# Kernel optimization log

Hardware: AMD Instinct MI355X
Metric: run time of the kernel (lower is better)

Reference implementation:

```python
import jax, jax.numpy as jnp
import numpy as np

NEG = -1e30
EPS = 1e-10


def setup_inputs() -> dict:
    key = jax.random.key(0)
    ks = jax.random.split(key, 8)
    N, D, W = 200000, 256, 128
    B = 64
    s = 0.02  # keep linear outputs well-scaled
    return {
        "node_features": jax.random.normal(ks[0], (N, D), jnp.float32),
        "node_tiers": jax.random.randint(ks[1], (N,), 0, 3, jnp.int32),
        "query": jax.random.normal(ks[2], (B, D), jnp.float32),
        "W_mu": jax.random.normal(ks[3], (W, D), jnp.float32) * s,
        "b_mu": jnp.zeros((W,), jnp.float32),
        "W_lv": jax.random.normal(ks[4], (W, D), jnp.float32) * s,
        "b_lv": jnp.zeros((W,), jnp.float32),
        "W_dec": jax.random.normal(ks[5], (D, W), jnp.float32) * s,
        "b_dec": jnp.zeros((D,), jnp.float32),
        "top_k": 16,
    }


def reference(node_features, node_tiers, query, W_mu, b_mu, W_lv, b_lv, W_dec, b_dec, top_k):
    # tiers: 0=hot, 1=warm, 2=cold
    warm = node_tiers == 1            # [N]
    cold = node_tiers == 2            # [N]

    # --- compress_warm_nodes (eval mode: z = mu) ---
    mu = node_features @ W_mu.T + b_mu          # [N, W]
    logvar = node_features @ W_lv.T + b_lv      # [N, W]
    dec = mu @ W_dec.T + b_dec                  # [N, D]
    new_features = jnp.where(warm[:, None], dec, node_features)

    kl_terms = -0.5 * (1.0 + logvar - mu * mu - jnp.exp(logvar))  # [N, W]
    n_warm = jnp.maximum(jnp.sum(warm), 1)
    kl_loss = jnp.sum(jnp.where(warm[:, None], kl_terms, 0.0)) / (n_warm * kl_terms.shape[1])

    # --- retrieve_from_cold: cosine sim + topk + gather ---
    qn = query / (jnp.linalg.norm(query, axis=-1, keepdims=True) + EPS)          # [B, D]
    fn = new_features / (jnp.linalg.norm(new_features, axis=-1, keepdims=True) + EPS)  # [N, D]
    sim = qn @ fn.T                                                              # [B, N]
    sim = jnp.where(cold[None, :], sim, NEG)
    top_sim, top_idx = jax.lax.top_k(sim, top_k)                                 # [B, k]
    retrieved = new_features[top_idx]                                            # [B, k, D]

    return new_features, kl_loss, retrieved, top_idx
```

## Files before the change

### kernel.cpp

```cpp
#include <hip/hip_runtime.h>
#include <math.h>

#define D 256
#define WDIM 128
#define EPSN 1e-10f
#define CHUNK 2048
#define C2 2048

typedef __attribute__((ext_vector_type(8))) short short8v;
typedef __attribute__((ext_vector_type(4))) float f32x4;

#define XPAD 264
#define MPAD 136

__device__ __forceinline__ unsigned short bf16_rne(float f) {
    unsigned u = __float_as_uint(f);
    u += 0x7fffu + ((u >> 16) & 1u);
    return (unsigned short)(u >> 16);
}
__device__ __forceinline__ float bf16_tof(unsigned short h) {
    return __uint_as_float(((unsigned)h) << 16);
}
__device__ __forceinline__ void split2(float f, unsigned short& h, unsigned short& l) {
    h = bf16_rne(f);
    l = bf16_rne(f - bf16_tof(h));
}

__global__ void k_init(int* cnt) {
    if (threadIdx.x == 0) { cnt[0] = 0; cnt[1] = 0; ((float*)cnt)[2] = 0.0f; }
}

__global__ __launch_bounds__(256) void k_wconv(const float* __restrict__ Wmu,
                                               const float* __restrict__ Wlv,
                                               const float* __restrict__ Wdec,
                                               unsigned short* __restrict__ wcat_h,
                                               unsigned short* __restrict__ wcat_l,
                                               unsigned short* __restrict__ wdec_h,
                                               unsigned short* __restrict__ wdec_l) {
    int i = blockIdx.x * 256 + threadIdx.x;
    if (i < 65536) {
        float v = (i < 32768) ? Wmu[i] : Wlv[i - 32768];
        unsigned short h, l; split2(v, h, l);
        wcat_h[i] = h; wcat_l[i] = l;
    } else if (i < 98304) {
        int j = i - 65536;
        unsigned short h, l; split2(Wdec[j], h, l);
        wdec_h[j] = h; wdec_l[j] = l;
    }
}

__global__ __launch_bounds__(256) void k_copy_norm(const float* __restrict__ x,
                                                   float* __restrict__ outF,
                                                   float* __restrict__ rowinv, int N) {
    int wid = threadIdx.x >> 6, lane = threadIdx.x & 63;
    int row = blockIdx.x * 4 + wid;
    if (row >= N) return;
    float4 v = ((const float4*)(x + (size_t)row * D))[lane];
    ((float4*)(outF + (size_t)row * D))[lane] = v;
    float s = v.x * v.x + v.y * v.y + v.z * v.z + v.w * v.w;
    #pragma unroll
    for (int m = 32; m; m >>= 1) s += __shfl_xor(s, m, 64);
    if (lane == 0) rowinv[row] = 1.0f / (sqrtf(s) + EPSN);
}

__global__ __launch_bounds__(256) void k_classify(const int* __restrict__ tiers, int* cnt,
                                                  int* __restrict__ warm_idx,
                                                  int* __restrict__ cold_idx, int N) {
    int i = blockIdx.x * 256 + threadIdx.x;
    bool w = false, c = false;
    if (i < N) { int t = tiers[i]; w = (t == 1); c = (t == 2); }
    unsigned long long mw = __ballot(w);
    unsigned long long mc = __ballot(c);
    int lane = threadIdx.x & 63;
    unsigned long long ltmask = (lane == 0) ? 0ULL : (~0ULL >> (64 - lane));
    int pw = __popcll(mw & ltmask);
    int pc = __popcll(mc & ltmask);
    int cw = __popcll(mw), cc = __popcll(mc);
    int bw = 0, bc = 0;
    if (lane == 0) {
        if (cw) bw = atomicAdd(&cnt[0], cw);
        if (cc) bc = atomicAdd(&cnt[1], cc);
    }
    bw = __shfl(bw, 0, 64);
    bc = __shfl(bc, 0, 64);
    if (w) warm_idx[bw + pw] = i;
    if (c) cold_idx[bc + pc] = i;
}

__global__ __launch_bounds__(256) void k_qnorm(const float* __restrict__ q,
                                               float* __restrict__ qn, int B) {
    int wid = threadIdx.x >> 6, lane = threadIdx.x & 63;
    int row = blockIdx.x * 4 + wid;
    if (row >= B) return;
    float4 v = ((const float4*)(q + (size_t)row * D))[lane];
    float s = v.x * v.x + v.y * v.y + v.z * v.z + v.w * v.w;
    #pragma unroll
    for (int m = 32; m; m >>= 1) s += __shfl_xor(s, m, 64);
    float inv = 1.0f / (sqrtf(s) + EPSN);
    float4 o = make_float4(v.x * inv, v.y * inv, v.z * inv, v.w * inv);
    ((float4*)(qn + (size_t)row * D))[lane] = o;
}

__global__ __launch_bounds__(256) void k_warm(const float* __restrict__ x,
        const unsigned short* __restrict__ wcat_h, const unsigned short* __restrict__ wcat_l,
        const unsigned short* __restrict__ wdec_h, const unsigned short* __restrict__ wdec_l,
        const float* __restrict__ bmu, const float* __restrict__ blv,
        const float* __restrict__ bdec,
        const int* __restrict__ warm_idx, const int* cnt,
        float* __restrict__ outF, float* klacc) {
    __shared__ __align__(16) unsigned short SM[2 * 64 * XPAD];
    __shared__ float klbuf[4];
    unsigned short* XH = SM;
    unsigned short* XL = SM + 64 * XPAD;
    int nw = cnt[0];
    int base = blockIdx.x * 64;
    if (base >= nw) return;
    int m = min(64, nw - base);
    int tid = threadIdx.x;
    for (int i = tid; i < 64 * 64; i += 256) {
        int r = i >> 6, c4 = i & 63;
        float4 v = make_float4(0.f, 0.f, 0.f, 0.f);
        if (r < m) v = ((const float4*)(x + (size_t)warm_idx[base + r] * D))[c4];
        unsigned short h0, h1, h2, h3, l0, l1, l2, l3;
        split2(v.x, h0, l0); split2(v.y, h1, l1); split2(v.z, h2, l2); split2(v.w, h3, l3);
        *(ushort4*)&XH[r * XPAD + c4 * 4] = make_ushort4(h0, h1, h2, h3);
        *(ushort4*)&XL[r * XPAD + c4 * 4] = make_ushort4(l0, l1, l2, l3);
    }
    __syncthreads();

    int w = tid >> 6, lane = tid & 63;
    int lm = lane & 15, lk = (lane >> 4) * 8;
    int rowbase = w * 16;
    f32x4 zero; zero[0] = 0.f; zero[1] = 0.f; zero[2] = 0.f; zero[3] = 0.f;

    f32x4 acc[16];
    #pragma unroll
    for (int n = 0; n < 16; ++n) acc[n] = zero;
    const unsigned short* ah_p = &XH[(rowbase + lm) * XPAD];
    const unsigned short* al_p = &XL[(rowbase + lm) * XPAD];
    for (int ks = 0; ks < 8; ++ks) {
        int kk = ks * 32 + lk;
        short8v ah = *(const short8v*)&ah_p[kk];
        short8v al = *(const short8v*)&al_p[kk];
        #pragma unroll
        for (int n = 0; n < 16; ++n) {
            size_t roff = ((size_t)(n * 16 + lm) << 8) + kk;
            short8v bh = *(const short8v*)(wcat_h + roff);
            short8v bl = *(const short8v*)(wcat_l + roff);
            acc[n] = __builtin_amdgcn_mfma_f32_16x16x32_bf16(ah, bh, acc[n], 0, 0, 0);
            acc[n] = __builtin_amdgcn_mfma_f32_16x16x32_bf16(al, bh, acc[n], 0, 0, 0);
            acc[n] = __builtin_amdgcn_mfma_f32_16x16x32_bf16(ah, bl, acc[n], 0, 0, 0);
        }
    }

    float kll = 0.f;
    int r4 = (lane >> 4) * 4;
    #pragma unroll
    for (int n = 0; n < 8; ++n) {
        float bm = bmu[n * 16 + lm];
        float bl_ = blv[n * 16 + lm];
        #pragma unroll
        for (int rg = 0; rg < 4; ++rg) {
            float mu = acc[n][rg] + bm;
            float lv = acc[n + 8][rg] + bl_;
            acc[n][rg] = mu;
            int rl = rowbase + r4 + rg;
            if (rl < m) kll += -0.5f * (1.f + lv - mu * mu - __expf(lv));
        }
    }
    #pragma unroll
    for (int s = 32; s; s >>= 1) kll += __shfl_xor(kll, s, 64);
    if (lane == 0) klbuf[w] = kll;
    __syncthreads();
    if (tid == 0) atomicAdd(klacc, klbuf[0] + klbuf[1] + klbuf[2] + klbuf[3]);

    unsigned short* MUH = SM;
    unsigned short* MUL = SM + 64 * MPAD;
    #pragma unroll
    for (int n = 0; n < 8; ++n) {
        #pragma unroll
        for (int rg = 0; rg < 4; ++rg) {
            int rl = rowbase + r4 + rg;
            unsigned short h, l;
            split2(acc[n][rg], h, l);
            MUH[rl * MPAD + n * 16 + lm] = h;
            MUL[rl * MPAD + n * 16 + lm] = l;
        }
    }
    __syncthreads();

    f32x4 acc2[16];
    #pragma unroll
    for (int n = 0; n < 16; ++n) acc2[n] = zero;
    const unsigned short* mh_p = &MUH[(rowbase + lm) * MPAD];
    const unsigned short* ml_p = &MUL[(rowbase + lm) * MPAD];
    for (int ks = 0; ks < 4; ++ks) {
        int kk = ks * 32 + lk;
        short8v ah = *(const short8v*)&mh_p[kk];
        short8v al = *(const short8v*)&ml_p[kk];
        #pragma unroll
        for (int n = 0; n < 16; ++n) {
            size_t roff = (size_t)(n * 16 + lm) * WDIM + kk;
            short8v bh = *(const short8v*)(wdec_h + roff);
            short8v bl = *(const short8v*)(wdec_l + roff);
            acc2[n] = __builtin_amdgcn_mfma_f32_16x16x32_bf16(ah, bh, acc2[n], 0, 0, 0);
            acc2[n] = __builtin_amdgcn_mfma_f32_16x16x32_bf16(al, bh, acc2[n], 0, 0, 0);
            acc2[n] = __builtin_amdgcn_mfma_f32_16x16x32_bf16(ah, bl, acc2[n], 0, 0, 0);
        }
    }

    int gidx[4];
    #pragma unroll
    for (int rg = 0; rg < 4; ++rg) {
        int rl = rowbase + r4 + rg;
        gidx[rg] = (rl < m) ? warm_idx[base + rl] : -1;
    }
    #pragma unroll
    for (int n = 0; n < 16; ++n) {
        float bd = bdec[n * 16 + lm];
        #pragma unroll
        for (int rg = 0; rg < 4; ++rg) {
            if (gidx[rg] >= 0)
                outF[(size_t)gidx[rg] * D + n * 16 + lm] = acc2[n][rg] + bd;
        }
    }
}

__global__ __launch_bounds__(256) void k_sim(const float* __restrict__ x,
                                             const float* __restrict__ qn,
                                             const int* __restrict__ cold_idx,
                                             const float* __restrict__ rowinv, const int* cnt,
                                             float* __restrict__ simC) {
    __shared__ float xs[64][256];
    int nc = cnt[1];
    int base = blockIdx.x * 64;
    if (base >= nc) return;
    int m = min(64, nc - base);
    int tid = threadIdx.x;
    for (int i = tid; i < 64 * 64; i += 256) {
        int r = i >> 6, c4 = i & 63;
        float4 v = make_float4(0.f, 0.f, 0.f, 0.f);
        if (r < m) v = ((const float4*)(x + (size_t)cold_idx[base + r] * D))[c4];
        *(float4*)&xs[r][c4 * 4] = v;
    }
    __syncthreads();
    int qg = tid & 15, rg = tid >> 4;
    int q0 = qg * 4, r0 = rg * 4;
    float acc[4][4] = {{0}};
    for (int k4 = 0; k4 < 64; ++k4) {
        float4 xv[4];
        #pragma unroll
        for (int i = 0; i < 4; ++i) xv[i] = *(const float4*)&xs[r0 + i][k4 * 4];
        #pragma unroll
        for (int j = 0; j < 4; ++j) {
            float4 qv = ((const float4*)(qn + (size_t)(q0 + j) * D))[k4];
            #pragma unroll
            for (int i = 0; i < 4; ++i)
                acc[i][j] += xv[i].x * qv.x + xv[i].y * qv.y + xv[i].z * qv.z + xv[i].w * qv.w;
        }
    }
    #pragma unroll
    for (int i = 0; i < 4; ++i) {
        int r = r0 + i;
        if (r < m) {
            float inv = rowinv[cold_idx[base + r]];
            #pragma unroll
            for (int j = 0; j < 4; ++j)
                simC[(size_t)(q0 + j) * nc + base + r] = acc[i][j] * inv;
        }
    }
}

__device__ __forceinline__ unsigned long long mkkey(float v, int gi) {
    unsigned int b = __float_as_uint(v);
    b = (b & 0x80000000u) ? ~b : (b | 0x80000000u);
    return ((unsigned long long)b << 32) | (unsigned int)(~gi);
}

#define CE(a, b) { unsigned long long _hi = (a) >= (b) ? (a) : (b); \
                   unsigned long long _lo = (a) >= (b) ? (b) : (a); \
                   (a) = _hi; (b) = _lo; }

__global__ __launch_bounds__(256) void k_top1(const float* __restrict__ simC,
                                              const int* __restrict__ cold_idx,
                                              const int* cnt, int Mmax,
                                              unsigned long long* __restrict__ cand) {
    __shared__ unsigned long long P0[256 * 17];
    __shared__ unsigned long long P1[128 * 17];
    int nc = cnt[1];
    int c = blockIdx.x, q = blockIdx.y;
    int base = c * CHUNK;
    if (base >= nc) return;
    int tid = threadIdx.x;
    const float* srow = simC + (size_t)q * nc;
    #define LOADK(s) ((base + tid + (s)*256 < nc) \
        ? mkkey(srow[base + tid + (s)*256], cold_idx[base + tid + (s)*256]) : 0ULL)
    unsigned long long k0 = LOADK(0), k1 = LOADK(1), k2 = LOADK(2), k3 = LOADK(3);
    unsigned long long k4 = LOADK(4), k5 = LOADK(5), k6 = LOADK(6), k7 = LOADK(7);
    #undef LOADK
    CE(k0,k1) CE(k2,k3) CE(k4,k5) CE(k6,k7)
    CE(k0,k2) CE(k1,k3) CE(k4,k6) CE(k5,k7)
    CE(k1,k2) CE(k5,k6)
    CE(k0,k4) CE(k1,k5) CE(k2,k6) CE(k3,k7)
    CE(k2,k4) CE(k3,k5)
    CE(k1,k2) CE(k3,k4) CE(k5,k6)
    unsigned long long* L = P0 + tid * 17;
    L[0]=k0; L[1]=k1; L[2]=k2; L[3]=k3; L[4]=k4; L[5]=k5; L[6]=k6; L[7]=k7;
    L[8]=0; L[9]=0; L[10]=0; L[11]=0; L[12]=0; L[13]=0; L[14]=0; L[15]=0;
    __syncthreads();
    unsigned long long* src = P0;
    unsigned long long* dst = P1;
    int nl = 256;
    while (nl > 1) {
        int half = nl >> 1;
        if (tid < half) {
            unsigned long long* A  = src + (2 * tid) * 17;
            unsigned long long* Bp = src + (2 * tid + 1) * 17;
            unsigned long long* O  = dst + tid * 17;
            int i = 0, j = 0;
            #pragma unroll
            for (int t = 0; t < 16; ++t) {
                unsigned long long ka = A[i], kb = Bp[j];
                bool ta = ka >= kb;
                O[t] = ta ? ka : kb;
                i += ta ? 1 : 0;
                j += ta ? 0 : 1;
            }
        }
        __syncthreads();
        unsigned long long* tmp = src; src = dst; dst = tmp;
        nl = half;
    }
    if (tid < 16) cand[((size_t)q * Mmax + c) * 16 + tid] = src[tid];
}

__global__ __launch_bounds__(256) void k_top2(const unsigned long long* __restrict__ cand,
                                              const int* cnt, int Mmax,
                                              const float* __restrict__ newF,
                                              float* __restrict__ outRetr,
                                              float* __restrict__ outIdx) {
    __shared__ unsigned long long K[C2];
    int q = blockIdx.x, tid = threadIdx.x;
    int nc = cnt[1];
    int M = (nc + CHUNK - 1) / CHUNK; if (M > Mmax) M = Mmax;
    int C = M * 16;
    for (int i = tid; i < C2; i += 256)
        K[i] = (i < C) ? cand[(size_t)q * Mmax * 16 + i] : 0ULL;
    __syncthreads();
    for (int kk = 2; kk <= C2; kk <<= 1) {
        for (int jj = kk >> 1; jj > 0; jj >>= 1) {
            for (int idx = tid; idx < C2; idx += 256) {
                int p = idx ^ jj;
                if (p > idx) {
                    bool dirDesc = ((idx & kk) == 0);
                    unsigned long long a = K[idx], b = K[p];
                    bool sw = dirDesc ? (a < b) : (a > b);
                    if (sw) { K[idx] = b; K[p] = a; }
                }
            }
            __syncthreads();
        }
    }
    if (tid < 16) {
        int gi = (int)(~(unsigned int)(K[tid] & 0xffffffffULL));
        outIdx[q * 16 + tid] = (float)gi;
    }
    for (int i = tid; i < 16 * D; i += 256) {
        int r = i >> 8, cc = i & 255;
        int gi = (int)(~(unsigned int)(K[r] & 0xffffffffULL));
        outRetr[(size_t)q * 16 * D + i] = newF[(size_t)gi * D + cc];
    }
}

__global__ void k_klfin(const int* cnt, float* outKl, int Wk) {
    float kl = ((const float*)cnt)[2];
    int nw = cnt[0]; if (nw < 1) nw = 1;
    *outKl = kl / ((float)nw * (float)Wk);
}

extern "C" void kernel_launch(void* const* d_in, const int* in_sizes, int n_in,
                              void* d_out, int out_size, void* d_ws, size_t ws_size,
                              hipStream_t stream) {
    (void)n_in; (void)out_size; (void)ws_size;
    const float* x    = (const float*)d_in[0];
    const int*   tier = (const int*)d_in[1];
    const float* qry  = (const float*)d_in[2];
    const float* Wmu  = (const float*)d_in[3];
    const float* bmu  = (const float*)d_in[4];
    const float* Wlv  = (const float*)d_in[5];
    const float* blv  = (const float*)d_in[6];
    const float* Wdec = (const float*)d_in[7];
    const float* bdec = (const float*)d_in[8];
    int N = in_sizes[0] / D;
    int B = in_sizes[2] / D;
    int Wk = in_sizes[4];
    int Mmax = (N + CHUNK - 1) / CHUNK;

    float* outF    = (float*)d_out;
    float* outKl   = outF + (size_t)N * D;
    float* outRetr = outKl + 1;
    float* outIdx  = outRetr + (size_t)B * 16 * D;

    char* ws = (char*)d_ws;
    int*   cnt      = (int*)ws;
    int*   warm_idx = (int*)(ws + 256);
    int*   cold_idx = warm_idx + N;
    float* rowinv   = (float*)(cold_idx + N);
    float* qn       = rowinv + N;
    unsigned long long* cand = (unsigned long long*)(qn + (size_t)B * D);
    unsigned short* wcat_h = (unsigned short*)(cand + (size_t)B * Mmax * 16);
    unsigned short* wcat_l = wcat_h + 256 * 256;
    unsigned short* wdec_h = wcat_l + 256 * 256;
    unsigned short* wdec_l = wdec_h + 256 * WDIM;
    float* simC     = (float*)(wdec_l + 256 * WDIM);

    k_init<<<1, 64, 0, stream>>>(cnt);
    k_wconv<<<384, 256, 0, stream>>>(Wmu, Wlv, Wdec, wcat_h, wcat_l, wdec_h, wdec_l);
    k_copy_norm<<<(N + 3) / 4, 256, 0, stream>>>(x, outF, rowinv, N);
    k_classify<<<(N + 255) / 256, 256, 0, stream>>>(tier, cnt, warm_idx, cold_idx, N);
    k_qnorm<<<(B + 3) / 4, 256, 0, stream>>>(qry, qn, B);
    k_warm<<<(N + 63) / 64, 256, 0, stream>>>(x, wcat_h, wcat_l, wdec_h, wdec_l,
                                              bmu, blv, bdec, warm_idx, cnt,
                                              outF, (float*)cnt + 2);
    k_sim<<<(N + 63) / 64, 256, 0, stream>>>(x, qn, cold_idx, rowinv, cnt, simC);
    k_top1<<<dim3(Mmax, B), 256, 0, stream>>>(simC, cold_idx, cnt, Mmax, cand);
    k_top2<<<B, 256, 0, stream>>>(cand, cnt, Mmax, outF, outRetr, outIdx);
    k_klfin<<<1, 1, 0, stream>>>(cnt, outKl, Wk);
}
```

Baseline: 1.010 ms.

## Repartition warm VAE GEMM across waves by output columns with fragment-packed weights

Each wave in the warm-node kernel used to cover 16 rows and all output columns, so every wave loaded the full weight matrices from global memory. Now each wave covers all 64 rows but only a quarter of the output column tiles, which cuts per-block weight traffic by four. The weights are pre-packed into MFMA fragment order so each lane loads them with one coalesced 16-byte read. Warm indices are cached in shared memory for the scatter. The cost is more LDS reads of the A operand per wave and a more complex layout in the weight-conversion kernel.

New measurement: 845.9 us. 1.19x faster.

```diff
diff --git a/kernel.cpp b/kernel.cpp
--- a/kernel.cpp
+++ b/kernel.cpp
@@ -39,12 +39,18 @@
                                                unsigned short* __restrict__ wdec_l) {
     int i = blockIdx.x * 256 + threadIdx.x;
     if (i < 65536) {
-        float v = (i < 32768) ? Wmu[i] : Wlv[i - 32768];
+        int e = i & 7, lane = (i >> 3) & 63, ks = (i >> 9) & 7, n = i >> 12;
+        int row = n * 16 + (lane & 15);
+        int k = ks * 32 + ((lane >> 4) << 3) + e;
+        float v = (row < 128) ? Wmu[row * 256 + k] : Wlv[(row - 128) * 256 + k];
         unsigned short h, l; split2(v, h, l);
         wcat_h[i] = h; wcat_l[i] = l;
     } else if (i < 98304) {
         int j = i - 65536;
-        unsigned short h, l; split2(Wdec[j], h, l);
+        int e = j & 7, lane = (j >> 3) & 63, ks = (j >> 9) & 3, n = j >> 11;
+        int row = n * 16 + (lane & 15);
+        int k = ks * 32 + ((lane >> 4) << 3) + e;
+        unsigned short h, l; split2(Wdec[row * 128 + k], h, l);
         wdec_h[j] = h; wdec_l[j] = l;
     }
 }
@@ -110,6 +116,7 @@
         float* __restrict__ outF, float* klacc) {
     __shared__ __align__(16) unsigned short SM[2 * 64 * XPAD];
     __shared__ float klbuf[4];
+    __shared__ int widx[64];
     unsigned short* XH = SM;
     unsigned short* XL = SM + 64 * XPAD;
     int nw = cnt[0];
@@ -117,6 +124,7 @@
     if (base >= nw) return;
     int m = min(64, nw - base);
     int tid = threadIdx.x;
+    if (tid < 64) widx[tid] = (tid < m) ? warm_idx[base + tid] : -1;
     for (int i = tid; i < 64 * 64; i += 256) {
         int r = i >> 6, c4 = i & 63;
         float4 v = make_float4(0.f, 0.f, 0.f, 0.f);
@@ -129,43 +137,53 @@
     __syncthreads();
 
     int w = tid >> 6, lane = tid & 63;
-    int lm = lane & 15, lk = (lane >> 4) * 8;
-    int rowbase = w * 16;
+    int lm = lane & 15, hi = lane >> 4;
+    int lk = hi * 8, r4 = hi * 4;
     f32x4 zero; zero[0] = 0.f; zero[1] = 0.f; zero[2] = 0.f; zero[3] = 0.f;
 
-    f32x4 acc[16];
-    #pragma unroll
-    for (int n = 0; n < 16; ++n) acc[n] = zero;
-    const unsigned short* ah_p = &XH[(rowbase + lm) * XPAD];
-    const unsigned short* al_p = &XL[(rowbase + lm) * XPAD];
+    f32x4 acc[4][4];
+    #pragma unroll
+    for (int t = 0; t < 4; ++t)
+        #pragma unroll
+        for (int j = 0; j < 4; ++j) acc[t][j] = zero;
     for (int ks = 0; ks < 8; ++ks) {
         int kk = ks * 32 + lk;
-        short8v ah = *(const short8v*)&ah_p[kk];
-        short8v al = *(const short8v*)&al_p[kk];
-        #pragma unroll
-        for (int n = 0; n < 16; ++n) {
-            size_t roff = ((size_t)(n * 16 + lm) << 8) + kk;
-            short8v bh = *(const short8v*)(wcat_h + roff);
-            short8v bl = *(const short8v*)(wcat_l + roff);
-            acc[n] = __builtin_amdgcn_mfma_f32_16x16x32_bf16(ah, bh, acc[n], 0, 0, 0);
-            acc[n] = __builtin_amdgcn_mfma_f32_16x16x32_bf16(al, bh, acc[n], 0, 0, 0);
-            acc[n] = __builtin_amdgcn_mfma_f32_16x16x32_bf16(ah, bl, acc[n], 0, 0, 0);
+        short8v ah[4], al[4];
+        #pragma unroll
+        for (int t = 0; t < 4; ++t) {
+            ah[t] = *(const short8v*)&XH[(t * 16 + lm) * XPAD + kk];
+            al[t] = *(const short8v*)&XL[(t * 16 + lm) * XPAD + kk];
+        }
+        #pragma unroll
+        for (int j = 0; j < 4; ++j) {
+            int fn = w + 4 * j;
+            short8v bh = ((const short8v*)wcat_h)[(fn * 8 + ks) * 64 + lane];
+            short8v bl = ((const short8v*)wcat_l)[(fn * 8 + ks) * 64 + lane];
+            #pragma unroll
+            for (int t = 0; t < 4; ++t) {
+                acc[t][j] = __builtin_amdgcn_mfma_f32_16x16x32_bf16(ah[t], bh, acc[t][j], 0, 0, 0);
+                acc[t][j] = __builtin_amdgcn_mfma_f32_16x16x32_bf16(al[t], bh, acc[t][j], 0, 0, 0);
+                acc[t][j] = __builtin_amdgcn_mfma_f32_16x16x32_bf16(ah[t], bl, acc[t][j], 0, 0, 0);
+            }
         }
     }
 
     float kll = 0.f;
-    int r4 = (lane >> 4) * 4;
-    #pragma unroll
-    for (int n = 0; n < 8; ++n) {
-        float bm = bmu[n * 16 + lm];
-        float bl_ = blv[n * 16 + lm];
-        #pragma unroll
-        for (int rg = 0; rg < 4; ++rg) {
-            float mu = acc[n][rg] + bm;
-            float lv = acc[n + 8][rg] + bl_;
-            acc[n][rg] = mu;
-            int rl = rowbase + r4 + rg;
-            if (rl < m) kll += -0.5f * (1.f + lv - mu * mu - __expf(lv));
+    #pragma unroll
+    for (int j = 0; j < 2; ++j) {
+        int fn = w + 4 * j;
+        float bm = bmu[fn * 16 + lm];
+        float bv = blv[fn * 16 + lm];
+        #pragma unroll
+        for (int t = 0; t < 4; ++t) {
+            #pragma unroll
+            for (int rg = 0; rg < 4; ++rg) {
+                float mu = acc[t][j][rg] + bm;
+                float lv = acc[t][j + 2][rg] + bv;
+                acc[t][j][rg] = mu;
+                int rl = t * 16 + r4 + rg;
+                if (rl < m) kll += -0.5f * (1.f + lv - mu * mu - __expf(lv));
+            }
         }
     }
     #pragma unroll
@@ -177,51 +195,64 @@
     unsigned short* MUH = SM;
     unsigned short* MUL = SM + 64 * MPAD;
     #pragma unroll
-    for (int n = 0; n < 8; ++n) {
-        #pragma unroll
-        for (int rg = 0; rg < 4; ++rg) {
-            int rl = rowbase + r4 + rg;
-            unsigned short h, l;
-            split2(acc[n][rg], h, l);
-            MUH[rl * MPAD + n * 16 + lm] = h;
-            MUL[rl * MPAD + n * 16 + lm] = l;
-        }
-    }
-    __syncthreads();
-
-    f32x4 acc2[16];
-    #pragma unroll
-    for (int n = 0; n < 16; ++n) acc2[n] = zero;
-    const unsigned short* mh_p = &MUH[(rowbase + lm) * MPAD];
-    const unsigned short* ml_p = &MUL[(rowbase + lm) * MPAD];
+    for (int j = 0; j < 2; ++j) {
+        int fn = w + 4 * j;
+        int col = fn * 16 + lm;
+        #pragma unroll
+        for (int t = 0; t < 4; ++t) {
+            #pragma unroll
+            for (int rg = 0; rg < 4; ++rg) {
+                int rl = t * 16 + r4 + rg;
+                unsigned short h, l;
+                split2(acc[t][j][rg], h, l);
+                MUH[rl * MPAD + col] = h;
+                MUL[rl * MPAD + col] = l;
+            }
+        }
+    }
+    __syncthreads();
+
+    f32x4 acc2[4][4];
+    #pragma unroll
+    for (int t = 0; t < 4; ++t)
+        #pragma unroll
+        for (int j = 0; j < 4; ++j) acc2[t][j] = zero;
     for (int ks = 0; ks < 4; ++ks) {
         int kk = ks * 32 + lk;
-        short8v ah = *(const short8v*)&mh_p[kk];
-        short8v al = *(const short8v*)&ml_p[kk];
-        #pragma unroll
-        for (int n = 0; n < 16; ++n) {
-            size_t roff = (size_t)(n * 16 + lm) * WDIM + kk;
-            short8v bh = *(const short8v*)(wdec_h + roff);
-            short8v bl = *(const short8v*)(wdec_l + roff);
-            acc2[n] = __builtin_amdgcn_mfma_f32_16x16x32_bf16(ah, bh, acc2[n], 0, 0, 0);
-            acc2[n] = __builtin_amdgcn_mfma_f32_16x16x32_bf16(al, bh, acc2[n], 0, 0, 0);
-            acc2[n] = __builtin_amdgcn_mfma_f32_16x16x32_bf16(ah, bl, acc2[n], 0, 0, 0);
-        }
-    }
-
-    int gidx[4];
-    #pragma unroll
-    for (int rg = 0; rg < 4; ++rg) {
-        int rl = rowbase + r4 + rg;
-        gidx[rg] = (rl < m) ? warm_idx[base + rl] : -1;
-    }
-    #pragma unroll
-    for (int n = 0; n < 16; ++n) {
-        float bd = bdec[n * 16 + lm];
-        #pragma unroll
-        for (int rg = 0; rg < 4; ++rg) {
-            if (gidx[rg] >= 0)
-                outF[(size_t)gidx[rg] * D + n * 16 + lm] = acc2[n][rg] + bd;
+        short8v ah[4], al[4];
+        #pragma unroll
+        for (int t = 0; t < 4; ++t) {
+            ah[t] = *(const short8v*)&MUH[(t * 16 + lm) * MPAD + kk];
+            al[t] = *(const short8v*)&MUL[(t * 16 + lm) * MPAD + kk];
+        }
+        #pragma unroll
+        for (int j = 0; j < 4; ++j) {
+            int fn = w * 4 + j;
+            short8v bh = ((const short8v*)wdec_h)[(fn * 4 + ks) * 64 + lane];
+            short8v bl = ((const short8v*)wdec_l)[(fn * 4 + ks) * 64 + lane];
+            #pragma unroll
+            for (int t = 0; t < 4; ++t) {
+                acc2[t][j] = __builtin_amdgcn_mfma_f32_16x16x32_bf16(ah[t], bh, acc2[t][j], 0, 0, 0);
+                acc2[t][j] = __builtin_amdgcn_mfma_f32_16x16x32_bf16(al[t], bh, acc2[t][j], 0, 0, 0);
+                acc2[t][j] = __builtin_amdgcn_mfma_f32_16x16x32_bf16(ah[t], bl, acc2[t][j], 0, 0, 0);
+            }
+        }
+    }
+
+    #pragma unroll
+    for (int j = 0; j < 4; ++j) {
+        int fn = w * 4 + j;
+        int col = fn * 16 + lm;
+        float bd = bdec[col];
+        #pragma unroll
+        for (int t = 0; t < 4; ++t) {
+            #pragma unroll
+            for (int rg = 0; rg < 4; ++rg) {
+                int rl = t * 16 + r4 + rg;
+                int gi = widx[rl];
+                if (gi >= 0)
+                    outF[(size_t)gi * D + col] = acc2[t][j][rg] + bd;
+            }
         }
     }
 }
```
